# Performance work log

Measured on AMD Instinct MI355X. Metric: run time of the kernel, lower is better.

The kernel has to match this reference:

```python
import jax, jax.numpy as jnp
import numpy as np

DEPTH = 3
UNITS = 512
EMBED = 64
CHARS = 55        # chars_num + 3
PATH_NUM = 8192
DEC_EMBED = PATH_NUM // 4  # 2048
B, T_IN, T_OUT = 64, 128, 128


def _lstm_cell(x, h, c, Wx, Wh, b):
    # Keras LSTMCell gate order: i, f, g (candidate), o
    z = x @ Wx + h @ Wh + b            # [B, 4U]
    i, f, g, o = jnp.split(z, 4, axis=-1)
    i = jax.nn.sigmoid(i)
    f = jax.nn.sigmoid(f)
    g = jnp.tanh(g)
    o = jax.nn.sigmoid(o)
    c2 = f * c + i * g
    h2 = o * jnp.tanh(c2)
    return h2, c2


def _run_stack(x_seq, init_states, Wd, bd, Wx, Wh, b):
    # x_seq: [T, B, E]; init_states: (h [D,B,U], c [D,B,U])
    # Per timestep: Dense(relu) -> 3 stacked LSTM cells.
    def step(carry, xt):
        h, c = carry
        inp = jax.nn.relu(xt @ Wd + bd)          # [B, U]
        hs, cs = [], []
        for l in range(DEPTH):
            h2, c2 = _lstm_cell(inp, h[l], c[l], Wx[l], Wh[l], b[l])
            hs.append(h2)
            cs.append(c2)
            inp = h2
        return (jnp.stack(hs), jnp.stack(cs)), inp
    (h, c), outs = jax.lax.scan(step, init_states, x_seq)
    return (h, c), outs                           # outs: [T, B, U]


def setup_inputs() -> dict:
    key = jax.random.key(0)
    ks = jax.random.split(key, 20)
    s = 0.02
    d = {}
    d["inputs"] = jax.random.randint(ks[0], (B, T_IN), 0, CHARS, dtype=jnp.int64)
    d["targets"] = jax.random.randint(ks[1], (B, T_OUT), 0, PATH_NUM, dtype=jnp.int64)
    d["input_embed"] = jax.random.normal(ks[2], (CHARS, EMBED), jnp.float32) * s
    d["enc_Wd"] = jax.random.normal(ks[3], (EMBED, UNITS), jnp.float32) * s
    d["enc_bd"] = jnp.zeros((UNITS,), jnp.float32)
    d["enc_Wx"] = jax.random.normal(ks[4], (DEPTH, UNITS, 4 * UNITS), jnp.float32) * s
    d["enc_Wh"] = jax.random.normal(ks[5], (DEPTH, UNITS, 4 * UNITS), jnp.float32) * s
    d["enc_b"] = jnp.zeros((DEPTH, 4 * UNITS), jnp.float32)
    d["dec_embed"] = jax.random.normal(ks[6], (PATH_NUM, DEC_EMBED), jnp.float32) * s
    d["dec_Wd"] = jax.random.normal(ks[7], (DEC_EMBED, UNITS), jnp.float32) * s
    d["dec_bd"] = jnp.zeros((UNITS,), jnp.float32)
    d["dec_Wx"] = jax.random.normal(ks[8], (DEPTH, UNITS, 4 * UNITS), jnp.float32) * s
    d["dec_Wh"] = jax.random.normal(ks[9], (DEPTH, UNITS, 4 * UNITS), jnp.float32) * s
    d["dec_b"] = jnp.zeros((DEPTH, 4 * UNITS), jnp.float32)
    d["out_W1"] = jax.random.normal(ks[10], (UNITS, 4 * UNITS), jnp.float32) * s
    d["out_b1"] = jnp.zeros((4 * UNITS,), jnp.float32)
    d["out_W2"] = jax.random.normal(ks[11], (4 * UNITS, PATH_NUM), jnp.float32) * s
    d["out_b2"] = jnp.zeros((PATH_NUM,), jnp.float32)
    return d


def reference(inputs, targets, input_embed, enc_Wd, enc_bd, enc_Wx, enc_Wh, enc_b,
              dec_embed, dec_Wd, dec_bd, dec_Wx, dec_Wh, dec_b,
              out_W1, out_b1, out_W2, out_b2):
    b = inputs.shape[0]
    zero = jnp.zeros((DEPTH, b, UNITS), jnp.float32)
    # Encoder: embed -> per-step Dense(relu) + 3-layer stacked LSTM
    x = input_embed[inputs]                       # [B, T_in, E]
    states, _ = _run_stack(x.transpose(1, 0, 2), (zero, zero),
                           enc_Wd, enc_bd, enc_Wx, enc_Wh, enc_b)
    # Decoder (teacher forcing): states continue from encoder
    t = dec_embed[targets]                        # [B, T_out, 2048]
    _, dec_outs = _run_stack(t.transpose(1, 0, 2), states,
                             dec_Wd, dec_bd, dec_Wx, dec_Wh, dec_b)
    # Output head: Dense(4U, relu) -> Dense(path_num, relu); no softmax in training path
    h1 = jax.nn.relu(dec_outs @ out_W1 + out_b1)  # [T, B, 4U]
    logits = jax.nn.relu(h1 @ out_W2 + out_b2)    # [T, B, path_num]
    return logits.transpose(1, 0, 2)              # [B, T_out, path_num]
```

## Files before the change

kernel.cpp:

```cpp
#include <hip/hip_runtime.h>

typedef unsigned short ushort_t;
typedef unsigned long long u64_t;
typedef __attribute__((ext_vector_type(8))) short short8;
typedef __attribute__((ext_vector_type(4))) float floatx4;

#define TT 128
#define UNITS 512
#define EMBED 64
#define PATHN 8192
#define DECE 2048
#define MROWS 8192

__device__ __forceinline__ float bf2f(ushort_t u) {
  union { unsigned int i; float f; } v;
  v.i = ((unsigned int)u) << 16;
  return v.f;
}
__device__ __forceinline__ ushort_t f2bf(float f) {
  union { float f; unsigned int i; } v;
  v.f = f;
  unsigned int x = v.i;
  x += 0x7fffu + ((x >> 16) & 1u);
  return (ushort_t)(x >> 16);
}
__device__ __forceinline__ float loadF(const void* p, size_t i, bool f32) {
  return f32 ? ((const float*)p)[i] : bf2f(((const ushort_t*)p)[i]);
}
__device__ __forceinline__ int loadI(const void* p, size_t i, bool i64) {
  return i64 ? (int)((const long long*)p)[i] : ((const int*)p)[i];
}

__global__ void detect_mode(const void* __restrict__ emb, const void* __restrict__ tgt,
                            int* __restrict__ mode) {
  __shared__ int crazy, nz;
  if (threadIdx.x == 0) { crazy = 0; nz = 0; }
  __syncthreads();
  int c = 0;
  for (int i = threadIdx.x; i < 2048; i += 256) {
    ushort_t u = ((const ushort_t*)emb)[i];
    int e = (u >> 7) & 0xff;
    if (e > 0x90) c++;
  }
  if (c) atomicAdd(&crazy, c);
  if (threadIdx.x < 32) {
    int v = ((const int*)tgt)[threadIdx.x * 2 + 1];
    if (v != 0) atomicAdd(&nz, 1);
  }
  __syncthreads();
  if (threadIdx.x == 0) {
    mode[0] = (crazy > 16) ? 1 : 0;
    mode[1] = (nz == 0) ? 1 : 0;
  }
}

__global__ void gather_enc(const int* __restrict__ mode, const void* __restrict__ inputs,
                           const void* __restrict__ emb, ushort_t* __restrict__ out) {
  const bool f32 = mode[0] != 0, i64 = mode[1] != 0;
  int tid = blockIdx.x * blockDim.x + threadIdx.x;
  int m = tid >> 3, part = tid & 7;
  int b = m & 63, t = m >> 6;
  int ch = loadI(inputs, (size_t)b * TT + t, i64);
  size_t src = (size_t)ch * EMBED + part * 8;
  ushort_t tmp[8];
  if (f32) {
#pragma unroll
    for (int j = 0; j < 8; j++) tmp[j] = f2bf(((const float*)emb)[src + j]);
  } else {
    *(short8*)tmp = *(const short8*)((const ushort_t*)emb + src);
  }
  *(short8*)(out + (size_t)m * EMBED + part * 8) = *(short8*)tmp;
}

__global__ void gather_dec(const int* __restrict__ mode, const void* __restrict__ targets,
                           const void* __restrict__ emb, ushort_t* __restrict__ out) {
  const bool f32 = mode[0] != 0, i64 = mode[1] != 0;
  int tid = blockIdx.x * blockDim.x + threadIdx.x;
  int m = tid >> 8, part = tid & 255;
  int b = m & 63, t = m >> 6;
  int p = loadI(targets, (size_t)b * TT + t, i64);
  size_t src = (size_t)p * DECE + part * 8;
  ushort_t tmp[8];
  if (f32) {
#pragma unroll
    for (int j = 0; j < 8; j++) tmp[j] = f2bf(((const float*)emb)[src + j]);
  } else {
    *(short8*)tmp = *(const short8*)((const ushort_t*)emb + src);
  }
  *(short8*)(out + (size_t)m * DECE + part * 8) = *(short8*)tmp;
}

__global__ void transpose_elems(const int* __restrict__ mode, const void* __restrict__ in,
                                size_t eo, ushort_t* __restrict__ out, int R, int C) {
  const bool f32 = mode[0] != 0;
  __shared__ ushort_t tl[32][33];
  int c0 = blockIdx.x * 32, r0 = blockIdx.y * 32;
  int x = threadIdx.x & 31, y4 = threadIdx.x >> 5;
#pragma unroll
  for (int i = 0; i < 4; i++) {
    int y = y4 + i * 8;
    tl[y][x] = f2bf(loadF(in, eo + (size_t)(r0 + y) * C + (c0 + x), f32));
  }
  __syncthreads();
#pragma unroll
  for (int i = 0; i < 4; i++) {
    int y = y4 + i * 8;
    out[(size_t)(c0 + y) * R + (r0 + x)] = tl[x][y];
  }
}

template <int RELU, int BIAS, int TSTORE>
__global__ __launch_bounds__(256) void gemm_bt(const int* __restrict__ mode,
                                               const ushort_t* __restrict__ A,
                                               const ushort_t* __restrict__ Bt,
                                               const void* __restrict__ bias,
                                               void* __restrict__ Cp, int M, int N, int K) {
  const bool f32 = mode[0] != 0;
  __shared__ __align__(16) ushort_t As[128 * 40];
  __shared__ __align__(16) ushort_t Bs[128 * 40];
  const int tid = threadIdx.x;
  const int lane = tid & 63, wv = tid >> 6;
  const int quad = lane >> 4, l16 = lane & 15;
  const int wrow = (wv & 1) * 64, wcol = (wv >> 1) * 64;
  floatx4 acc[4][4] = {};
  const int srow = tid >> 1, scol = (tid & 1) * 16;
  const ushort_t* Ag = A + (size_t)(blockIdx.y * 128 + srow) * K + scol;
  const ushort_t* Bg = Bt + (size_t)(blockIdx.x * 128 + srow) * K + scol;
  ushort_t* AsW = &As[srow * 40 + scol];
  ushort_t* BsW = &Bs[srow * 40 + scol];
  for (int k0 = 0; k0 < K; k0 += 32) {
    short8 a0 = *(const short8*)(Ag + k0);
    short8 a1 = *(const short8*)(Ag + k0 + 8);
    short8 b0 = *(const short8*)(Bg + k0);
    short8 b1 = *(const short8*)(Bg + k0 + 8);
    __syncthreads();
    *(short8*)AsW = a0;
    *(short8*)(AsW + 8) = a1;
    *(short8*)BsW = b0;
    *(short8*)(BsW + 8) = b1;
    __syncthreads();
    short8 af[4], bfr[4];
#pragma unroll
    for (int i = 0; i < 4; i++) af[i] = *(const short8*)&As[(wrow + i * 16 + l16) * 40 + quad * 8];
#pragma unroll
    for (int j = 0; j < 4; j++) bfr[j] = *(const short8*)&Bs[(wcol + j * 16 + l16) * 40 + quad * 8];
#pragma unroll
    for (int i = 0; i < 4; i++)
#pragma unroll
      for (int j = 0; j < 4; j++)
        acc[i][j] = __builtin_amdgcn_mfma_f32_16x16x32_bf16(af[i], bfr[j], acc[i][j], 0, 0, 0);
  }
  const int mbase = blockIdx.y * 128 + wrow;
  const int nbase = blockIdx.x * 128 + wcol;
#pragma unroll
  for (int j = 0; j < 4; j++) {
    int col = nbase + j * 16 + l16;
    float bv = BIAS ? loadF(bias, col, f32) : 0.0f;
#pragma unroll
    for (int i = 0; i < 4; i++) {
#pragma unroll
      for (int r = 0; r < 4; r++) {
        int row = mbase + i * 16 + quad * 4 + r;
        float v = acc[i][j][r] + bv;
        if (RELU) v = fmaxf(v, 0.0f);
        if (TSTORE) {
          size_t o = (size_t)(row & 63) * ((size_t)TT * PATHN) + (size_t)(row >> 6) * PATHN + col;
          if (f32) ((float*)Cp)[o] = v;
          else ((ushort_t*)Cp)[o] = f2bf(v);
        } else {
          ((ushort_t*)Cp)[(size_t)row * N + col] = f2bf(v);
        }
      }
    }
  }
}

__device__ __forceinline__ short8 load_h16(const ushort_t* p) {
  union { u64_t q[2]; short8 v; } u;
  u.q[0] = __hip_atomic_load((const u64_t*)p, __ATOMIC_RELAXED, __HIP_MEMORY_SCOPE_AGENT);
  u.q[1] = __hip_atomic_load((const u64_t*)p + 1, __ATOMIC_RELAXED, __HIP_MEMORY_SCOPE_AGENT);
  return u.v;
}
__device__ __forceinline__ void store_h(ushort_t* p, ushort_t v) {
  __hip_atomic_store(p, v, __ATOMIC_RELAXED, __HIP_MEMORY_SCOPE_AGENT);
}
__device__ __forceinline__ int* fgrp(int* flags, int T, int l) {
  return flags + ((size_t)(T * 3 + l) << 10);
}
__device__ __forceinline__ void wait_grp(const int* g1, const int* g2, int lane) {
  const int* p = ((lane < 32) ? g1 : g2) + (lane & 31) * 32;
  while (!__all(__hip_atomic_load(p, __ATOMIC_RELAXED, __HIP_MEMORY_SCOPE_AGENT) != 0)) {
  }
}

__global__ __launch_bounds__(256) void lstm_persist(
    const int* __restrict__ mode, int t0, int t1, const ushort_t* __restrict__ z1,
    const ushort_t* __restrict__ Wxt, const ushort_t* __restrict__ Wht,
    const void* __restrict__ bias, ushort_t* __restrict__ hbuf, float* __restrict__ cbuf,
    ushort_t* __restrict__ decouts, int* __restrict__ flags) {
  const bool f32 = mode[0] != 0;
  const int l = blockIdx.x >> 5;
  const int cb = blockIdx.x & 31;
  const int tid = threadIdx.x;
  const int lane = tid & 63, wv = tid >> 6;
  const int quad = lane >> 4, l16 = lane & 15;
  const int col = cb * 16 + l16;

  __shared__ __align__(16) ushort_t Wh_s[64 * 520];
  __shared__ __align__(16) ushort_t Wx_s[64 * 520];

  {
    const ushort_t* WhG = Wht + (size_t)l * 2048 * 512;
    const ushort_t* WxG = Wxt + (size_t)l * 2048 * 512;
    for (int i = tid; i < 64 * 64; i += 256) {
      int r = i >> 6, kc = (i & 63) << 3;
      int g = r >> 4, c = r & 15;
      size_t grow = (size_t)g * 512 + cb * 16 + c;
      *(short8*)&Wh_s[r * 520 + kc] = *(const short8*)&WhG[grow * 512 + kc];
      if (l > 0) *(short8*)&Wx_s[r * 520 + kc] = *(const short8*)&WxG[grow * 512 + kc];
    }
  }
  floatx4 creg;
#pragma unroll
  for (int r = 0; r < 4; r++)
    creg[r] = cbuf[((size_t)l * 64 + wv * 16 + quad * 4 + r) * 512 + col];
  const float bi = loadF(bias, l * 2048 + col, f32);
  const float bff = loadF(bias, l * 2048 + 512 + col, f32);
  const float bg = loadF(bias, l * 2048 + 1024 + col, f32);
  const float bo = loadF(bias, l * 2048 + 1536 + col, f32);
  __syncthreads();

  const int arow = wv * 16 + l16;
  const int koff = quad * 8;

  for (int T = t0; T < t1; ++T) {
    const int pw = T & 3, pr = (T - 1) & 3;
    if (T > 0) {
      if (wv == 0) {
        const int* g1 = fgrp(flags, T - 1, l);
        const int* g2 = (l < 2 && T >= 4) ? fgrp(flags, T - 4, l + 1) : g1;
        wait_grp(g1, g2, lane);
      }
      __syncthreads();
    }

    floatx4 acc[4] = {};
    {
      const ushort_t* hL = hbuf + ((size_t)pr * 3 + l) * 64 * 512 + (size_t)arow * 512 + koff;
#pragma unroll
      for (int k0 = 0; k0 < 512; k0 += 32) {
        short8 a = load_h16(hL + k0);
#pragma unroll
        for (int g = 0; g < 4; g++) {
          short8 b = *(const short8*)&Wh_s[(g * 16 + l16) * 520 + k0 + koff];
          acc[g] = __builtin_amdgcn_mfma_f32_16x16x32_bf16(a, b, acc[g], 0, 0, 0);
        }
      }
    }
    if (l > 0) {
      if (wv == 0) {
        const int* g = fgrp(flags, T, l - 1);
        wait_grp(g, g, lane);
      }
      __syncthreads();
      const ushort_t* hX = hbuf + ((size_t)pw * 3 + (l - 1)) * 64 * 512 + (size_t)arow * 512 + koff;
#pragma unroll
      for (int k0 = 0; k0 < 512; k0 += 32) {
        short8 a = load_h16(hX + k0);
#pragma unroll
        for (int g = 0; g < 4; g++) {
          short8 b = *(const short8*)&Wx_s[(g * 16 + l16) * 520 + k0 + koff];
          acc[g] = __builtin_amdgcn_mfma_f32_16x16x32_bf16(a, b, acc[g], 0, 0, 0);
        }
      }
    }
    ushort_t* hO = hbuf + ((size_t)pw * 3 + l) * 64 * 512;
#pragma unroll
    for (int r = 0; r < 4; r++) {
      int row = wv * 16 + quad * 4 + r;
      float zi = acc[0][r] + bi;
      float zf = acc[1][r] + bff;
      float zg = acc[2][r] + bg;
      float zo = acc[3][r] + bo;
      if (l == 0) {
        const ushort_t* zr = z1 + ((size_t)(T - t0) * 64 + row) * 2048;
        zi += bf2f(zr[col]);
        zf += bf2f(zr[512 + col]);
        zg += bf2f(zr[1024 + col]);
        zo += bf2f(zr[1536 + col]);
      }
      zi = fminf(fmaxf(zi, -30.f), 30.f);
      zf = fminf(fmaxf(zf, -30.f), 30.f);
      zg = fminf(fmaxf(zg, -30.f), 30.f);
      zo = fminf(fmaxf(zo, -30.f), 30.f);
      float iv = 1.0f / (1.0f + expf(-zi));
      float fv = 1.0f / (1.0f + expf(-zf));
      float gv = tanhf(zg);
      float ov = 1.0f / (1.0f + expf(-zo));
      float cn = fv * creg[r] + iv * gv;
      creg[r] = cn;
      float hv = ov * tanhf(cn);
      store_h(&hO[(size_t)row * 512 + col], f2bf(hv));
      if (decouts && l == 2) decouts[((size_t)(T - t0) * 64 + row) * 512 + col] = f2bf(hv);
    }
    __syncthreads();
    if (tid == 0)
      __hip_atomic_store(fgrp(flags, T, l) + cb * 32, 1, __ATOMIC_RELAXED,
                         __HIP_MEMORY_SCOPE_AGENT);
  }
#pragma unroll
  for (int r = 0; r < 4; r++)
    cbuf[((size_t)l * 64 + wv * 16 + quad * 4 + r) * 512 + col] = creg[r];
}

extern "C" void kernel_launch(void* const* d_in, const int* in_sizes, int n_in, void* d_out,
                              int out_size, void* d_ws, size_t ws_size, hipStream_t stream) {
  const void* inputs = d_in[0];
  const void* targets = d_in[1];
  const void* input_embed = d_in[2];
  const void* enc_Wd = d_in[3];
  const void* enc_bd = d_in[4];
  const void* enc_Wx = d_in[5];
  const void* enc_Wh = d_in[6];
  const void* enc_b = d_in[7];
  const void* dec_embed = d_in[8];
  const void* dec_Wd = d_in[9];
  const void* dec_bd = d_in[10];
  const void* dec_Wx = d_in[11];
  const void* dec_Wh = d_in[12];
  const void* dec_b = d_in[13];
  const void* out_W1 = d_in[14];
  const void* out_b1 = d_in[15];
  const void* out_W2 = d_in[16];
  const void* out_b2 = d_in[17];

  char* ws = (char*)d_ws;
  size_t off = 0;
  auto alloc = [&](size_t bytes) {
    void* p = ws + off;
    off += (bytes + 255) & ~(size_t)255;
    return p;
  };
  int* mode = (int*)alloc(256);
  int* flags = (int*)alloc((size_t)768 * 1024 * 4);
  ushort_t* encWd_t = (ushort_t*)alloc((size_t)512 * 64 * 2);
  ushort_t* encWx_t = (ushort_t*)alloc((size_t)3 * 2048 * 512 * 2);
  ushort_t* encWh_t = (ushort_t*)alloc((size_t)3 * 2048 * 512 * 2);
  ushort_t* decWd_t = (ushort_t*)alloc((size_t)512 * 2048 * 2);
  ushort_t* decWx_t = (ushort_t*)alloc((size_t)3 * 2048 * 512 * 2);
  ushort_t* decWh_t = (ushort_t*)alloc((size_t)3 * 2048 * 512 * 2);
  ushort_t* outW1_t = (ushort_t*)alloc((size_t)2048 * 512 * 2);
  ushort_t* encx = (ushort_t*)alloc((size_t)MROWS * EMBED * 2);
  ushort_t* encin = (ushort_t*)alloc((size_t)MROWS * 512 * 2);
  ushort_t* dect = (ushort_t*)alloc((size_t)MROWS * 2048 * 2);
  ushort_t* decin = (ushort_t*)alloc((size_t)MROWS * 512 * 2);
  ushort_t* zbuf = (ushort_t*)alloc((size_t)MROWS * 2048 * 2);
  ushort_t* hbuf = (ushort_t*)alloc((size_t)4 * 3 * 64 * 512 * 2);
  float* cbuf = (float*)alloc((size_t)3 * 64 * 512 * 4);
  ushort_t* decouts = (ushort_t*)alloc((size_t)MROWS * 512 * 2);
  ushort_t* h1 = (ushort_t*)alloc((size_t)MROWS * 2048 * 2);
  ushort_t* W2t = dect;

  hipMemsetAsync(hbuf, 0, (size_t)4 * 3 * 64 * 512 * 2, stream);
  hipMemsetAsync(cbuf, 0, (size_t)3 * 64 * 512 * 4, stream);
  hipMemsetAsync(flags, 0, (size_t)768 * 1024 * 4, stream);

  detect_mode<<<1, 256, 0, stream>>>(input_embed, targets, mode);

  gather_enc<<<256, 256, 0, stream>>>(mode, inputs, input_embed, encx);
  gather_dec<<<8192, 256, 0, stream>>>(mode, targets, dec_embed, dect);

  transpose_elems<<<dim3(16, 2), 256, 0, stream>>>(mode, enc_Wd, 0, encWd_t, 64, 512);
  for (int l = 0; l < 3; l++) {
    size_t eo = (size_t)l * 512 * 2048;
    size_t to = (size_t)l * 2048 * 512;
    transpose_elems<<<dim3(64, 16), 256, 0, stream>>>(mode, enc_Wx, eo, encWx_t + to, 512, 2048);
    transpose_elems<<<dim3(64, 16), 256, 0, stream>>>(mode, enc_Wh, eo, encWh_t + to, 512, 2048);
    transpose_elems<<<dim3(64, 16), 256, 0, stream>>>(mode, dec_Wx, eo, decWx_t + to, 512, 2048);
    transpose_elems<<<dim3(64, 16), 256, 0, stream>>>(mode, dec_Wh, eo, decWh_t + to, 512, 2048);
  }
  transpose_elems<<<dim3(16, 64), 256, 0, stream>>>(mode, dec_Wd, 0, decWd_t, 2048, 512);
  transpose_elems<<<dim3(64, 16), 256, 0, stream>>>(mode, out_W1, 0, outW1_t, 512, 2048);

  gemm_bt<1, 1, 0><<<dim3(4, 64), 256, 0, stream>>>(mode, encx, encWd_t, enc_bd, encin, MROWS, 512, 64);
  gemm_bt<0, 0, 0><<<dim3(16, 64), 256, 0, stream>>>(mode, encin, encWx_t, nullptr, zbuf, MROWS, 2048, 512);
  gemm_bt<1, 1, 0><<<dim3(4, 64), 256, 0, stream>>>(mode, dect, decWd_t, dec_bd, decin, MROWS, 512, 2048);
  transpose_elems<<<dim3(256, 64), 256, 0, stream>>>(mode, out_W2, 0, W2t, 2048, 8192);

  lstm_persist<<<96, 256, 0, stream>>>(mode, 0, 128, zbuf, encWx_t, encWh_t, enc_b, hbuf, cbuf,
                                       nullptr, flags);
  gemm_bt<0, 0, 0><<<dim3(16, 64), 256, 0, stream>>>(mode, decin, decWx_t, nullptr, zbuf, MROWS, 2048, 512);
  lstm_persist<<<96, 256, 0, stream>>>(mode, 128, 256, zbuf, decWx_t, decWh_t, dec_b, hbuf, cbuf,
                                       decouts, flags);

  gemm_bt<1, 1, 0><<<dim3(16, 64), 256, 0, stream>>>(mode, decouts, outW1_t, out_b1, h1, MROWS, 2048, 512);
  gemm_bt<1, 1, 1><<<dim3(64, 64), 256, 0, stream>>>(mode, h1, W2t, out_b2, d_out, MROWS, PATHN, 2048);
}
```

Baseline: 3.925 ms.

## Merge encoder/decoder LSTM into one persistent kernel with register-resident weights and K-split

Fuses the encoder and decoder persistent LSTM launches into a single 256-step launch. Cell state now stays in registers and no longer round-trips through a global buffer. Recurrent and input weights move from shared memory into per-wave registers, and each wave takes a K-slice of 128 instead of a row slice. Partial sums are reduced through shared memory, and the pointwise step writes packed 4-element h stores. The decoder input projection GEMM now runs before the LSTM into the h1 buffer. The trade-offs are an extra shared-memory reduction and sync per step, heavy register pressure, and a bounded spin-wait guard that could break out early.

```diff
diff --git a/kernel.cpp b/kernel.cpp
--- a/kernel.cpp
+++ b/kernel.cpp
@@ -3,6 +3,7 @@
 typedef unsigned short ushort_t;
 typedef unsigned long long u64_t;
 typedef __attribute__((ext_vector_type(8))) short short8;
+typedef __attribute__((ext_vector_type(4))) short bfx4;
 typedef __attribute__((ext_vector_type(4))) float floatx4;
 
 #define TT 128
@@ -181,22 +182,40 @@
   u.q[1] = __hip_atomic_load((const u64_t*)p + 1, __ATOMIC_RELAXED, __HIP_MEMORY_SCOPE_AGENT);
   return u.v;
 }
-__device__ __forceinline__ void store_h(ushort_t* p, ushort_t v) {
-  __hip_atomic_store(p, v, __ATOMIC_RELAXED, __HIP_MEMORY_SCOPE_AGENT);
-}
 __device__ __forceinline__ int* fgrp(int* flags, int T, int l) {
   return flags + ((size_t)(T * 3 + l) << 10);
 }
 __device__ __forceinline__ void wait_grp(const int* g1, const int* g2, int lane) {
   const int* p = ((lane < 32) ? g1 : g2) + (lane & 31) * 32;
+  int guard = 0;
   while (!__all(__hip_atomic_load(p, __ATOMIC_RELAXED, __HIP_MEMORY_SCOPE_AGENT) != 0)) {
-  }
-}
-
-__global__ __launch_bounds__(256) void lstm_persist(
-    const int* __restrict__ mode, int t0, int t1, const ushort_t* __restrict__ z1,
-    const ushort_t* __restrict__ Wxt, const ushort_t* __restrict__ Wht,
-    const void* __restrict__ bias, ushort_t* __restrict__ hbuf, float* __restrict__ cbuf,
+    if (++guard > 10000000) break;
+  }
+}
+
+#define LOADW(WHG, WXG, BIASP)                                                              \
+  {                                                                                         \
+    const ushort_t* _wh = (WHG) + (size_t)l * 2048 * 512;                                   \
+    const ushort_t* _wx = (WXG) + (size_t)l * 2048 * 512;                                   \
+    _Pragma("unroll") for (int g = 0; g < 4; g++) {                                         \
+      _Pragma("unroll") for (int kb = 0; kb < 4; kb++) {                                    \
+        size_t rr = (size_t)(g * 512 + cb * 16 + l16) * 512 + kbase + kb * 32 + quad * 8;   \
+        whf[g][kb] = *(const short8*)&_wh[rr];                                              \
+        if (l > 0) wxf[g][kb] = *(const short8*)&_wx[rr];                                   \
+      }                                                                                     \
+    }                                                                                       \
+    _Pragma("unroll") for (int g = 0; g < 4; g++) {                                         \
+      _Pragma("unroll") for (int j = 0; j < 4; j++)                                         \
+        bs[g][j] = loadF((BIASP), l * 2048 + g * 512 + col0 + j, f32);                      \
+    }                                                                                       \
+  }
+
+__global__ __launch_bounds__(256, 1) void lstm_persist(
+    const int* __restrict__ mode, const ushort_t* __restrict__ z1e,
+    const ushort_t* __restrict__ z1d, const ushort_t* __restrict__ WxtE,
+    const ushort_t* __restrict__ WhtE, const void* __restrict__ biasE,
+    const ushort_t* __restrict__ WxtD, const ushort_t* __restrict__ WhtD,
+    const void* __restrict__ biasD, ushort_t* __restrict__ hbuf,
     ushort_t* __restrict__ decouts, int* __restrict__ flags) {
   const bool f32 = mode[0] != 0;
   const int l = blockIdx.x >> 5;
@@ -204,37 +223,20 @@
   const int tid = threadIdx.x;
   const int lane = tid & 63, wv = tid >> 6;
   const int quad = lane >> 4, l16 = lane & 15;
-  const int col = cb * 16 + l16;
-
-  __shared__ __align__(16) ushort_t Wh_s[64 * 520];
-  __shared__ __align__(16) ushort_t Wx_s[64 * 520];
-
-  {
-    const ushort_t* WhG = Wht + (size_t)l * 2048 * 512;
-    const ushort_t* WxG = Wxt + (size_t)l * 2048 * 512;
-    for (int i = tid; i < 64 * 64; i += 256) {
-      int r = i >> 6, kc = (i & 63) << 3;
-      int g = r >> 4, c = r & 15;
-      size_t grow = (size_t)g * 512 + cb * 16 + c;
-      *(short8*)&Wh_s[r * 520 + kc] = *(const short8*)&WhG[grow * 512 + kc];
-      if (l > 0) *(short8*)&Wx_s[r * 520 + kc] = *(const short8*)&WxG[grow * 512 + kc];
-    }
-  }
-  floatx4 creg;
-#pragma unroll
-  for (int r = 0; r < 4; r++)
-    creg[r] = cbuf[((size_t)l * 64 + wv * 16 + quad * 4 + r) * 512 + col];
-  const float bi = loadF(bias, l * 2048 + col, f32);
-  const float bff = loadF(bias, l * 2048 + 512 + col, f32);
-  const float bg = loadF(bias, l * 2048 + 1024 + col, f32);
-  const float bo = loadF(bias, l * 2048 + 1536 + col, f32);
-  __syncthreads();
-
-  const int arow = wv * 16 + l16;
-  const int koff = quad * 8;
-
-  for (int T = t0; T < t1; ++T) {
-    const int pw = T & 3, pr = (T - 1) & 3;
+  const int kbase = wv * 128;
+  const int erow = tid >> 2;
+  const int ec = (tid & 3) * 4;
+  const int col0 = cb * 16 + ec;
+
+  __shared__ __align__(16) float zred[4][64][68];
+
+  short8 whf[4][4], wxf[4][4];
+  floatx4 bs[4];
+  LOADW(WhtE, WxtE, biasE);
+
+  floatx4 cstate = {};
+
+  for (int T = 0; T < 256; ++T) {
     if (T > 0) {
       if (wv == 0) {
         const int* g1 = fgrp(flags, T - 1, l);
@@ -243,74 +245,99 @@
       }
       __syncthreads();
     }
-
-    floatx4 acc[4] = {};
-    {
-      const ushort_t* hL = hbuf + ((size_t)pr * 3 + l) * 64 * 512 + (size_t)arow * 512 + koff;
-#pragma unroll
-      for (int k0 = 0; k0 < 512; k0 += 32) {
-        short8 a = load_h16(hL + k0);
-#pragma unroll
-        for (int g = 0; g < 4; g++) {
-          short8 b = *(const short8*)&Wh_s[(g * 16 + l16) * 520 + k0 + koff];
-          acc[g] = __builtin_amdgcn_mfma_f32_16x16x32_bf16(a, b, acc[g], 0, 0, 0);
-        }
+    if (T == TT) LOADW(WhtD, WxtD, biasD);
+
+    floatx4 acc[4][4] = {};
+    const ushort_t* hL = hbuf + ((size_t)((T - 1) & 3) * 3 + l) * 64 * 512;
+    short8 af[4][4];
+#pragma unroll
+    for (int i = 0; i < 4; i++)
+#pragma unroll
+      for (int kb = 0; kb < 4; kb++)
+        af[i][kb] = load_h16(hL + (size_t)(i * 16 + l16) * 512 + kbase + kb * 32 + quad * 8);
+    if (l > 0 && wv == 0) {
+      const int* g = fgrp(flags, T, l - 1);
+      wait_grp(g, g, lane);
+    }
+#pragma unroll
+    for (int kb = 0; kb < 4; kb++)
+#pragma unroll
+      for (int i = 0; i < 4; i++)
+#pragma unroll
+        for (int g = 0; g < 4; g++)
+          acc[i][g] =
+              __builtin_amdgcn_mfma_f32_16x16x32_bf16(af[i][kb], whf[g][kb], acc[i][g], 0, 0, 0);
+    if (l > 0) {
+      __syncthreads();
+      const ushort_t* hX = hbuf + ((size_t)(T & 3) * 3 + (l - 1)) * 64 * 512;
+#pragma unroll
+      for (int i = 0; i < 4; i++)
+#pragma unroll
+        for (int kb = 0; kb < 4; kb++)
+          af[i][kb] = load_h16(hX + (size_t)(i * 16 + l16) * 512 + kbase + kb * 32 + quad * 8);
+#pragma unroll
+      for (int kb = 0; kb < 4; kb++)
+#pragma unroll
+        for (int i = 0; i < 4; i++)
+#pragma unroll
+          for (int g = 0; g < 4; g++)
+            acc[i][g] =
+                __builtin_amdgcn_mfma_f32_16x16x32_bf16(af[i][kb], wxf[g][kb], acc[i][g], 0, 0, 0);
+    }
+#pragma unroll
+    for (int i = 0; i < 4; i++)
+#pragma unroll
+      for (int g = 0; g < 4; g++)
+#pragma unroll
+        for (int r = 0; r < 4; r++)
+          zred[wv][i * 16 + quad * 4 + r][g * 16 + l16] = acc[i][g][r];
+    __syncthreads();
+
+    ushort_t* hO = hbuf + ((size_t)(T & 3) * 3 + l) * 64 * 512;
+    floatx4 z[4];
+#pragma unroll
+    for (int g = 0; g < 4; g++) {
+      floatx4 s = *(const floatx4*)&zred[0][erow][g * 16 + ec];
+#pragma unroll
+      for (int w = 1; w < 4; w++) s += *(const floatx4*)&zred[w][erow][g * 16 + ec];
+      z[g] = s + bs[g];
+    }
+    if (l == 0) {
+      const ushort_t* zr = ((T < TT) ? z1e + ((size_t)T * 64 + erow) * 2048
+                                     : z1d + ((size_t)(T - TT) * 64 + erow) * 2048) +
+                           cb * 16 + ec;
+#pragma unroll
+      for (int g = 0; g < 4; g++) {
+        bfx4 v = *(const bfx4*)(zr + g * 512);
+#pragma unroll
+        for (int j = 0; j < 4; j++) z[g][j] += bf2f((ushort_t)v[j]);
       }
     }
-    if (l > 0) {
-      if (wv == 0) {
-        const int* g = fgrp(flags, T, l - 1);
-        wait_grp(g, g, lane);
-      }
-      __syncthreads();
-      const ushort_t* hX = hbuf + ((size_t)pw * 3 + (l - 1)) * 64 * 512 + (size_t)arow * 512 + koff;
-#pragma unroll
-      for (int k0 = 0; k0 < 512; k0 += 32) {
-        short8 a = load_h16(hX + k0);
-#pragma unroll
-        for (int g = 0; g < 4; g++) {
-          short8 b = *(const short8*)&Wx_s[(g * 16 + l16) * 520 + k0 + koff];
-          acc[g] = __builtin_amdgcn_mfma_f32_16x16x32_bf16(a, b, acc[g], 0, 0, 0);
-        }
-      }
-    }
-    ushort_t* hO = hbuf + ((size_t)pw * 3 + l) * 64 * 512;
-#pragma unroll
-    for (int r = 0; r < 4; r++) {
-      int row = wv * 16 + quad * 4 + r;
-      float zi = acc[0][r] + bi;
-      float zf = acc[1][r] + bff;
-      float zg = acc[2][r] + bg;
-      float zo = acc[3][r] + bo;
-      if (l == 0) {
-        const ushort_t* zr = z1 + ((size_t)(T - t0) * 64 + row) * 2048;
-        zi += bf2f(zr[col]);
-        zf += bf2f(zr[512 + col]);
-        zg += bf2f(zr[1024 + col]);
-        zo += bf2f(zr[1536 + col]);
-      }
-      zi = fminf(fmaxf(zi, -30.f), 30.f);
-      zf = fminf(fmaxf(zf, -30.f), 30.f);
-      zg = fminf(fmaxf(zg, -30.f), 30.f);
-      zo = fminf(fmaxf(zo, -30.f), 30.f);
+    union { ushort_t s[4]; u64_t q; } up;
+#pragma unroll
+    for (int j = 0; j < 4; j++) {
+      float zi = fminf(fmaxf(z[0][j], -30.f), 30.f);
+      float zf = fminf(fmaxf(z[1][j], -30.f), 30.f);
+      float zg = fminf(fmaxf(z[2][j], -30.f), 30.f);
+      float zo = fminf(fmaxf(z[3][j], -30.f), 30.f);
       float iv = 1.0f / (1.0f + expf(-zi));
       float fv = 1.0f / (1.0f + expf(-zf));
       float gv = tanhf(zg);
       float ov = 1.0f / (1.0f + expf(-zo));
-      float cn = fv * creg[r] + iv * gv;
-      creg[r] = cn;
-      float hv = ov * tanhf(cn);
-      store_h(&hO[(size_t)row * 512 + col], f2bf(hv));
-      if (decouts && l == 2) decouts[((size_t)(T - t0) * 64 + row) * 512 + col] = f2bf(hv);
-    }
+      float cn = fv * cstate[j] + iv * gv;
+      cstate[j] = cn;
+      up.s[j] = f2bf(ov * tanhf(cn));
+    }
+    __hip_atomic_store((u64_t*)(hO + (size_t)erow * 512 + col0), up.q, __ATOMIC_RELAXED,
+                       __HIP_MEMORY_SCOPE_AGENT);
+    if (l == 2 && T >= TT)
+      *(u64_t*)(decouts + ((size_t)(T - TT) * 64 + erow) * 512 + col0) = up.q;
+
     __syncthreads();
     if (tid == 0)
       __hip_atomic_store(fgrp(flags, T, l) + cb * 32, 1, __ATOMIC_RELAXED,
                          __HIP_MEMORY_SCOPE_AGENT);
   }
-#pragma unroll
-  for (int r = 0; r < 4; r++)
-    cbuf[((size_t)l * 64 + wv * 16 + quad * 4 + r) * 512 + col] = creg[r];
 }
 
 extern "C" void kernel_launch(void* const* d_in, const int* in_sizes, int n_in, void* d_out,
@@ -356,13 +383,11 @@
   ushort_t* decin = (ushort_t*)alloc((size_t)MROWS * 512 * 2);
   ushort_t* zbuf = (ushort_t*)alloc((size_t)MROWS * 2048 * 2);
   ushort_t* hbuf = (ushort_t*)alloc((size_t)4 * 3 * 64 * 512 * 2);
-  float* cbuf = (float*)alloc((size_t)3 * 64 * 512 * 4);
   ushort_t* decouts = (ushort_t*)alloc((size_t)MROWS * 512 * 2);
   ushort_t* h1 = (ushort_t*)alloc((size_t)MROWS * 2048 * 2);
   ushort_t* W2t = dect;
 
   hipMemsetAsync(hbuf, 0, (size_t)4 * 3 * 64 * 512 * 2, stream);
-  hipMemsetAsync(cbuf, 0, (size_t)3 * 64 * 512 * 4, stream);
   hipMemsetAsync(flags, 0, (size_t)768 * 1024 * 4, stream);
 
   detect_mode<<<1, 256, 0, stream>>>(input_embed, targets, mode);
@@ -385,13 +410,11 @@
   gemm_bt<1, 1, 0><<<dim3(4, 64), 256, 0, stream>>>(mode, encx, encWd_t, enc_bd, encin, MROWS, 512, 64);
   gemm_bt<0, 0, 0><<<dim3(16, 64), 256, 0, stream>>>(mode, encin, encWx_t, nullptr, zbuf, MROWS, 2048, 512);
   gemm_bt<1, 1, 0><<<dim3(4, 64), 256, 0, stream>>>(mode, dect, decWd_t, dec_bd, decin, MROWS, 512, 2048);
+  gemm_bt<0, 0, 0><<<dim3(16, 64), 256, 0, stream>>>(mode, decin, decWx_t, nullptr, h1, MROWS, 2048, 512);
   transpose_elems<<<dim3(256, 64), 256, 0, stream>>>(mode, out_W2, 0, W2t, 2048, 8192);
 
-  lstm_persist<<<96, 256, 0, stream>>>(mode, 0, 128, zbuf, encWx_t, encWh_t, enc_b, hbuf, cbuf,
-                                       nullptr, flags);
-  gemm_bt<0, 0, 0><<<dim3(16, 64), 256, 0, stream>>>(mode, decin, decWx_t, nullptr, zbuf, MROWS, 2048, 512);
-  lstm_persist<<<96, 256, 0, stream>>>(mode, 128, 256, zbuf, decWx_t, decWh_t, dec_b, hbuf, cbuf,
-                                       decouts, flags);
+  lstm_persist<<<96, 256, 0, stream>>>(mode, zbuf, h1, encWx_t, encWh_t, enc_b, decWx_t, decWh_t,
+                                       dec_b, hbuf, decouts, flags);
 
   gemm_bt<1, 1, 0><<<dim3(16, 64), 256, 0, stream>>>(mode, decouts, outW1_t, out_b1, h1, MROWS, 2048, 512);
   gemm_bt<1, 1, 1><<<dim3(64, 64), 256, 0, stream>>>(mode, h1, W2t, out_b2, d_out, MROWS, PATHN, 2048);
```

New measurement: 3.901 ms. About the same (-0.6%).
